# Kernel optimization log

Hardware: AMD Instinct MI355X
Metric: run time of the kernel (lower is better)

Reference implementation:

```python
import jax, jax.numpy as jnp
import numpy as np
from jax import lax

# --- config (matches init_kwargs) ---
D = 1024        # hidden_dim
H = 16          # num_heads
DH = D // H     # head dim
S = 5           # num_saccades
W = 128         # window_size
BK = 32         # block_size
TAU = 1.0       # gumbel temperature
DFF = 4 * D
EPS = 1e-5


def _ln(x, g, b):
    m = jnp.mean(x, axis=-1, keepdims=True)
    v = jnp.mean(jnp.square(x - m), axis=-1, keepdims=True)
    return (x - m) * lax.rsqrt(v + EPS) * g + b


def setup_inputs() -> dict:
    key = jax.random.key(0)
    ks = jax.random.split(key, 16)
    B, L = 4, 2048
    NB = L // BK
    sd = 0.02
    inp = {
        "hidden_states": jax.random.normal(ks[0], (B, L, D), jnp.float32),
        "gumbel_u": jax.random.uniform(ks[1], (S, B, NB), jnp.float32),
        "ln1_g": jnp.ones((D,), jnp.float32),
        "ln1_b": jnp.zeros((D,), jnp.float32),
        "ln2_g": jnp.ones((D,), jnp.float32),
        "ln2_b": jnp.zeros((D,), jnp.float32),
        "w_sal": jax.random.normal(ks[2], (D,), jnp.float32) * sd,
        "b_sal": jnp.zeros((), jnp.float32),
        "in_proj_w": jax.random.normal(ks[3], (3 * D, D), jnp.float32) * sd,
        "in_proj_b": jnp.zeros((3 * D,), jnp.float32),
        "out_proj_w": jax.random.normal(ks[4], (D, D), jnp.float32) * sd,
        "out_proj_b": jnp.zeros((D,), jnp.float32),
        "w_fc": jax.random.normal(ks[5], (D, DFF), jnp.float32) * sd,
        "b_fc": jnp.zeros((DFF,), jnp.float32),
        "w_proj": jax.random.normal(ks[6], (DFF, D), jnp.float32) * sd,
        "b_proj": jnp.zeros((D,), jnp.float32),
    }
    return inp


def reference(hidden_states, gumbel_u, ln1_g, ln1_b, ln2_g, ln2_b, w_sal, b_sal,
              in_proj_w, in_proj_b, out_proj_w, out_proj_b, w_fc, b_fc, w_proj, b_proj):
    x = hidden_states
    B, L, _ = x.shape
    NB = L // BK

    # ---- pre-norm ----
    h = _ln(x, ln1_g, ln1_b)

    # ---- peripheral map: mean-pool blocks, saliency logits ----
    blocks = h.reshape(B, NB, BK, D).mean(axis=2)          # (B, NB, D)
    logits = blocks @ w_sal + b_sal                        # (B, NB)

    # ---- gumbel-softmax hard block selection (straight-through) ----
    g = -jnp.log(-jnp.log(gumbel_u + 1e-9) + 1e-9)          # (S, B, NB)
    pert = (logits[None] + g) / TAU                         # (S, B, NB)
    p = jax.nn.softmax(pert, axis=-1)
    sel = jnp.argmax(pert, axis=-1)                         # (S, B) int
    w_soft = jnp.take_along_axis(p, sel[..., None], axis=-1)[..., 0]  # (S, B)
    scale = 1.0 + w_soft - lax.stop_gradient(w_soft)        # ST: fwd == 1

    # ---- gather fixation windows around selected block centers ----
    center = sel * BK + BK // 2
    start = jnp.clip(center - W // 2, 0, L - W)             # (S, B)
    idx = start[..., None] + jnp.arange(W)                  # (S, B, W)
    windows = h[jnp.arange(B)[None, :, None], idx, :]       # (S, B, W, D)
    windows = windows * scale[..., None, None]
    kv = windows.transpose(1, 0, 2, 3).reshape(B, S * W, D)  # (B, S*W, D)

    # ---- foveal MHA: queries = all tokens, keys/values = fixations ----
    wq, wk, wv = in_proj_w[:D], in_proj_w[D:2 * D], in_proj_w[2 * D:]
    bq, bk, bv = in_proj_b[:D], in_proj_b[D:2 * D], in_proj_b[2 * D:]
    q = (h @ wq.T + bq).reshape(B, L, H, DH)
    k = (kv @ wk.T + bk).reshape(B, S * W, H, DH)
    v = (kv @ wv.T + bv).reshape(B, S * W, H, DH)
    scores = jnp.einsum('blhd,bmhd->bhlm', q, k) / np.sqrt(DH).astype(np.float32)
    attn = jax.nn.softmax(scores, axis=-1)
    o = jnp.einsum('bhlm,bmhd->blhd', attn, v).reshape(B, L, D)
    o = o @ out_proj_w.T + out_proj_b

    x = x + o                                               # residual 1

    # ---- MLP (GPT-2: gelu-new) ----
    h2 = _ln(x, ln2_g, ln2_b)
    m = jax.nn.gelu(h2 @ w_fc + b_fc, approximate=True) @ w_proj + b_proj
    return x + m                                            # residual 2
```

## Files before the change

### kernel.cpp

```cpp
#include <hip/hip_runtime.h>

#define D_   1024
#define H_   16
#define DH_  64
#define S_   5
#define W_   128
#define BKB_ 32
#define DFF_ 4096
#define B_   4
#define L_   2048
#define NB_  64
#define SW_  (S_*W_)

typedef unsigned short u16;
typedef __attribute__((ext_vector_type(8))) short short8;
typedef __attribute__((ext_vector_type(4))) float floatx4;

__device__ __forceinline__ u16 f2bf(float f){
  unsigned int u = __float_as_uint(f);
  unsigned int r = 0x7fffu + ((u >> 16) & 1u);
  return (u16)((u + r) >> 16);
}

__device__ __forceinline__ void async_copy16(const u16* g, u16* lds){
  __builtin_amdgcn_global_load_lds(
      (const __attribute__((address_space(1))) void*)g,
      (__attribute__((address_space(3))) void*)lds, 16, 0, 0);
}

__device__ __forceinline__ float gelu_fast(float x){
  float u2 = 1.5957691216057308f * x * __builtin_fmaf(0.044715f, x*x, 1.0f);
  u2 = fminf(u2, 20.0f);
  float t = __expf(u2);
  return x * t * __builtin_amdgcn_rcpf(t + 1.0f);
}

__global__ void cast_f32_to_bf16(const float* __restrict__ in, u16* __restrict__ out, int n4){
  int i = blockIdx.x*256 + threadIdx.x;
  if (i < n4){
    float4 v = reinterpret_cast<const float4*>(in)[i];
    uint2 p;
    p.x = (unsigned)f2bf(v.x) | ((unsigned)f2bf(v.y) << 16);
    p.y = (unsigned)f2bf(v.z) | ((unsigned)f2bf(v.w) << 16);
    reinterpret_cast<uint2*>(out)[i] = p;
  }
}

__global__ void transpose_cast(const float* __restrict__ in, u16* __restrict__ out, int R, int C){
  __shared__ float t[32][33];
  int bx = blockIdx.x*32, by = blockIdx.y*32;
  int x = threadIdx.x & 31, y = threadIdx.x >> 5;
  #pragma unroll
  for (int i=0;i<4;i++)
    t[y + i*8][x] = in[(long long)(by + y + i*8)*C + bx + x];
  __syncthreads();
  #pragma unroll
  for (int i=0;i<4;i++)
    out[(long long)(bx + y + i*8)*R + by + x] = f2bf(t[x][y + i*8]);
}

template<bool ROWDOT>
__global__ __launch_bounds__(256) void ln_kernel(
    const float* __restrict__ x, const float* __restrict__ g, const float* __restrict__ b,
    const float* __restrict__ wsal, u16* __restrict__ out, float* __restrict__ logits)
{
  __shared__ float red[8];
  int row = blockIdx.x;
  int t = threadIdx.x;
  const float* xr = x + (long long)row*D_;
  float4 v = reinterpret_cast<const float4*>(xr)[t];
  float s  = v.x+v.y+v.z+v.w;
  float sq = v.x*v.x+v.y*v.y+v.z*v.z+v.w*v.w;
  #pragma unroll
  for (int m=32;m>=1;m>>=1){ s += __shfl_xor(s,m); sq += __shfl_xor(sq,m); }
  int wid = t>>6;
  if ((t&63)==0){ red[wid]=s; red[wid+4]=sq; }
  __syncthreads();
  s  = red[0]+red[1]+red[2]+red[3];
  sq = red[4]+red[5]+red[6]+red[7];
  float mean = s * (1.0f/D_);
  float var  = sq * (1.0f/D_) - mean*mean;
  float rstd = rsqrtf(fmaxf(var,0.0f) + 1e-5f);
  float4 gg = reinterpret_cast<const float4*>(g)[t];
  float4 bb = reinterpret_cast<const float4*>(b)[t];
  float h0 = (v.x-mean)*rstd*gg.x + bb.x;
  float h1 = (v.y-mean)*rstd*gg.y + bb.y;
  float h2 = (v.z-mean)*rstd*gg.z + bb.z;
  float h3 = (v.w-mean)*rstd*gg.w + bb.w;
  uint2 p;
  p.x = (unsigned)f2bf(h0) | ((unsigned)f2bf(h1) << 16);
  p.y = (unsigned)f2bf(h2) | ((unsigned)f2bf(h3) << 16);
  reinterpret_cast<uint2*>(out + (long long)row*D_)[t] = p;
  if (ROWDOT){
    float4 ww = reinterpret_cast<const float4*>(wsal)[t];
    float d = h0*ww.x + h1*ww.y + h2*ww.z + h3*ww.w;
    #pragma unroll
    for (int m=32;m>=1;m>>=1) d += __shfl_xor(d,m);
    __syncthreads();
    if ((t&63)==0) red[wid] = d;
    __syncthreads();
    if (t==0)
      atomicAdd(logits + (row>>5), (red[0]+red[1]+red[2]+red[3]) * (1.0f/BKB_));
  }
}

__global__ void select_kernel(const float* __restrict__ logits, const float* __restrict__ gum,
                              const float* __restrict__ bsal, int* __restrict__ start)
{
  int s = blockIdx.x >> 2, b = blockIdx.x & 3;
  int n = threadIdx.x;
  float u = gum[(s*B_ + b)*NB_ + n];
  float g = -logf(-logf(u + 1e-9f) + 1e-9f);
  float val = logits[b*NB_ + n] + bsal[0] + g;
  int idx = n;
  #pragma unroll
  for (int m=1;m<64;m<<=1){
    float ov = __shfl_xor(val, m);
    int   oi = __shfl_xor(idx, m);
    if (ov > val || (ov == val && oi < idx)) { val = ov; idx = oi; }
  }
  if (n==0){
    int c = idx*BKB_ + BKB_/2 - W_/2;
    c = c < 0 ? 0 : (c > (L_-W_) ? (L_-W_) : c);
    start[blockIdx.x] = c;
  }
}

__global__ void gather_kv(const u16* __restrict__ h, const int* __restrict__ start, u16* __restrict__ kv){
  int row = blockIdx.x;
  int b = row / SW_; int sw = row % SW_; int s = sw >> 7; int w = sw & 127;
  long long src = (long long)(b*L_ + start[s*B_ + b] + w)*D_;
  reinterpret_cast<uint2*>(kv + (long long)row*D_)[threadIdx.x] =
      reinterpret_cast<const uint2*>(h + src)[threadIdx.x];
}

template<int EPI>
__global__ __launch_bounds__(256) void gemm_bt(
    const u16* __restrict__ A, const u16* __restrict__ Bm,
    const float* __restrict__ bias, const float* __restrict__ res,
    void* __restrict__ Cout, void* __restrict__ Cout2, int M, int N, int K)
{
  __shared__ u16 As[2][128*32];
  __shared__ u16 Bs[2][128*32];
  const int tid = threadIdx.x;
  const int wave = tid>>6, lane = tid&63;
  const int wr = wave>>1, wc = wave&1;
  const int quad = lane>>4, l16 = lane&15;
  const int rowA0 = blockIdx.x*128;
  const int colB0 = blockIdx.y*128;
  const int r0  = tid>>2;
  const int cst = (tid&3) ^ ((tid>>2)&3);
  const u16* aP0 = A  + (long long)(rowA0 + r0     )*K + cst*8;
  const u16* aP1 = A  + (long long)(rowA0 + 64 + r0)*K + cst*8;
  const u16* bP0 = Bm + (long long)(colB0 + r0     )*K + cst*8;
  const u16* bP1 = Bm + (long long)(colB0 + 64 + r0)*K + cst*8;
  u16* ldsA = &As[0][0] + wave*512;
  u16* ldsB = &Bs[0][0] + wave*512;
  const int swq = l16 & 3;
  floatx4 acc[4][4];
  #pragma unroll
  for (int i=0;i<4;i++)
    #pragma unroll
    for (int j=0;j<4;j++) acc[i][j] = (floatx4)0.0f;

  const int T = K >> 5;
  async_copy16(aP0, ldsA);
  async_copy16(aP1, ldsA + 2048);
  async_copy16(bP0, ldsB);
  async_copy16(bP1, ldsB + 2048);

  for (int t=0; t<T; ++t){
    __syncthreads();
    if (t+1 < T){
      const int nb = (t+1)&1, ko = (t+1)<<5;
      async_copy16(aP0 + ko, ldsA + nb*4096);
      async_copy16(aP1 + ko, ldsA + nb*4096 + 2048);
      async_copy16(bP0 + ko, ldsB + nb*4096);
      async_copy16(bP1 + ko, ldsB + nb*4096 + 2048);
    }
    const u16* Ab = &As[t&1][0];
    const u16* Bb = &Bs[t&1][0];
    short8 af[4], bfv[4];
    #pragma unroll
    for (int i=0;i<4;i++){
      const int co = ((quad ^ swq))*8;
      af[i]  = *reinterpret_cast<const short8*>(Ab + (wr*64 + i*16 + l16)*32 + co);
      bfv[i] = *reinterpret_cast<const short8*>(Bb + (wc*64 + i*16 + l16)*32 + co);
    }
    #pragma unroll
    for (int i=0;i<4;i++)
      #pragma unroll
      for (int j=0;j<4;j++)
        acc[i][j] = __builtin_amdgcn_mfma_f32_16x16x32_bf16(af[i], bfv[j], acc[i][j], 0,0,0);
  }

  #pragma unroll
  for (int i=0;i<4;i++){
    #pragma unroll
    for (int j=0;j<4;j++){
      int row0 = rowA0 + wr*64 + i*16 + quad*4;
      int col  = colB0 + wc*64 + j*16 + l16;
      float bc = bias[col];
      if (EPI==3){
        if (col < 1024){
          #pragma unroll
          for (int r=0;r<4;r++)
            ((u16*)Cout)[(long long)(row0+r)*1024 + col] = f2bf(acc[i][j][r] + bc);
        } else {
          int vcol = col - 1024;
          int h = vcol >> 6, dh = vcol & 63;
          int b = row0 / SW_, mm = row0 % SW_;
          uint2 pk;
          pk.x = (unsigned)f2bf(acc[i][j][0]+bc) | ((unsigned)f2bf(acc[i][j][1]+bc) << 16);
          pk.y = (unsigned)f2bf(acc[i][j][2]+bc) | ((unsigned)f2bf(acc[i][j][3]+bc) << 16);
          *reinterpret_cast<uint2*>((u16*)Cout2 + ((long long)((b*H_ + h)*DH_ + dh))*SW_ + mm) = pk;
        }
      } else {
        #pragma unroll
        for (int r=0;r<4;r++){
          long long cidx = (long long)(row0+r)*N + col;
          float val = acc[i][j][r] + bc;
          if (EPI==0)      ((u16*)Cout)[cidx] = f2bf(val);
          else if (EPI==1) ((u16*)Cout)[cidx] = f2bf(gelu_fast(val));
          else             ((float*)Cout)[cidx] = val + res[cidx];
        }
      }
    }
  }
}

__global__ __launch_bounds__(256) void attn_kernel(
    const u16* __restrict__ q, const u16* __restrict__ k, const u16* __restrict__ vT,
    u16* __restrict__ o)
{
  const int bh = blockIdx.x;
  const int b = bh >> 4, h = bh & 15;
  const int tid = threadIdx.x;
  const int wave = tid >> 6, lane = tid & 63;
  const int quad = lane >> 4, l16 = lane & 15;
  const int qrow0 = blockIdx.y*64 + wave*16;

  __shared__ u16 Ks[64*64];
  __shared__ u16 Vs[64*64];
  __shared__ u16 Ps[4][16*72];

  const u16* qp = q + ((long long)(b*L_ + qrow0 + l16)*D_ + h*DH_ + quad*8);
  short8 qf0 = *reinterpret_cast<const short8*>(qp);
  short8 qf1 = *reinterpret_cast<const short8*>(qp + 32);

  floatx4 Oacc[4];
  #pragma unroll
  for (int dt=0;dt<4;dt++) Oacc[dt] = (floatx4)0.0f;
  float lsum = 0.0f;

  const int srow = lane >> 3;
  const int scol = ((lane & 7) ^ srow) * 8;
  const int sw16 = l16 & 7;
  u16* PsW = Ps[wave];

  for (int mt=0; mt<SW_/64; ++mt){
    const int m0 = mt*64;
    __syncthreads();
    #pragma unroll
    for (int c=0;c<2;c++){
      int rk = wave*8 + c*32 + srow;
      async_copy16(k  + ((long long)(b*SW_ + m0 + rk)*D_ + h*DH_) + scol,
                   Ks + (wave*8 + c*32)*64);
      async_copy16(vT + ((long long)(bh*DH_ + rk)*SW_ + m0) + scol,
                   Vs + (wave*8 + c*32)*64);
    }
    __syncthreads();

    #pragma unroll
    for (int sub=0; sub<4; ++sub){
      short8 kf0 = *reinterpret_cast<const short8*>(Ks + (sub*16+l16)*64 + ((quad  ) ^ sw16)*8);
      short8 kf1 = *reinterpret_cast<const short8*>(Ks + (sub*16+l16)*64 + ((quad+4) ^ sw16)*8);
      floatx4 st = (floatx4)0.0f;
      st = __builtin_amdgcn_mfma_f32_16x16x32_bf16(kf0, qf0, st, 0,0,0);
      st = __builtin_amdgcn_mfma_f32_16x16x32_bf16(kf1, qf1, st, 0,0,0);
      float p0 = __expf(st[0]*0.125f);
      float p1 = __expf(st[1]*0.125f);
      float p2 = __expf(st[2]*0.125f);
      float p3 = __expf(st[3]*0.125f);
      lsum += (p0+p1) + (p2+p3);
      uint2 pk;
      pk.x = (unsigned)f2bf(p0) | ((unsigned)f2bf(p1) << 16);
      pk.y = (unsigned)f2bf(p2) | ((unsigned)f2bf(p3) << 16);
      *reinterpret_cast<uint2*>(PsW + l16*72 + sub*16 + quad*4) = pk;
    }

    short8 pf0 = *reinterpret_cast<const short8*>(PsW + l16*72 + quad*8);
    short8 pf1 = *reinterpret_cast<const short8*>(PsW + l16*72 + 32 + quad*8);

    #pragma unroll
    for (int dt=0; dt<4; ++dt){
      short8 vf0 = *reinterpret_cast<const short8*>(Vs + (dt*16+l16)*64 + ((quad  ) ^ sw16)*8);
      short8 vf1 = *reinterpret_cast<const short8*>(Vs + (dt*16+l16)*64 + ((quad+4) ^ sw16)*8);
      Oacc[dt] = __builtin_amdgcn_mfma_f32_16x16x32_bf16(pf0, vf0, Oacc[dt], 0,0,0);
      Oacc[dt] = __builtin_amdgcn_mfma_f32_16x16x32_bf16(pf1, vf1, Oacc[dt], 0,0,0);
    }
  }

  lsum += __shfl_xor(lsum, 16);
  lsum += __shfl_xor(lsum, 32);

  #pragma unroll
  for (int r=0;r<4;r++){
    float linv = 1.0f / __shfl(lsum, quad*4 + r);
    int qrow = qrow0 + quad*4 + r;
    #pragma unroll
    for (int dt=0;dt<4;dt++)
      o[((long long)(b*L_ + qrow))*D_ + h*DH_ + dt*16 + l16] = f2bf(Oacc[dt][r]*linv);
  }
}

extern "C" void kernel_launch(void* const* d_in, const int* in_sizes, int n_in,
                              void* d_out, int out_size, void* d_ws, size_t ws_size,
                              hipStream_t stream)
{
  const float* x     = (const float*)d_in[0];
  const float* gum   = (const float*)d_in[1];
  const float* ln1g  = (const float*)d_in[2];
  const float* ln1b  = (const float*)d_in[3];
  const float* ln2g  = (const float*)d_in[4];
  const float* ln2b  = (const float*)d_in[5];
  const float* wsal  = (const float*)d_in[6];
  const float* bsal  = (const float*)d_in[7];
  const float* inpw  = (const float*)d_in[8];
  const float* inpb  = (const float*)d_in[9];
  const float* outw  = (const float*)d_in[10];
  const float* outb  = (const float*)d_in[11];
  const float* wfc   = (const float*)d_in[12];
  const float* bfc   = (const float*)d_in[13];
  const float* wproj = (const float*)d_in[14];
  const float* bproj = (const float*)d_in[15];
  float* outp = (float*)d_out;
  char* ws = (char*)d_ws;

  const size_t BLD2 = (size_t)B_*L_*D_*2;
  size_t off = 0;
  auto alloc = [&](size_t n){ char* p = ws + off; off += (n + 1023) & ~(size_t)1023; return p; };
  u16*  WfcT   = (u16*)alloc((size_t)DFF_*D_*2);
  u16*  WprojT = (u16*)alloc((size_t)D_*DFF_*2);
  float* x2    = (float*)alloc((size_t)B_*L_*D_*4);
  float* logits= (float*)alloc(B_*NB_*4);
  int*  startb = (int*)alloc(S_*B_*4);
  char* regA = ws + off;
  size_t o1 = 0;
  auto alloc1 = [&](size_t n){ char* p = regA + o1; o1 += (n + 1023) & ~(size_t)1023; return p; };
  u16* h_buf = (u16*)alloc1(BLD2);
  u16* Wqkv  = (u16*)alloc1((size_t)3*D_*D_*2);
  u16* Wout  = (u16*)alloc1((size_t)D_*D_*2);
  u16* qb    = (u16*)alloc1(BLD2);
  u16* kvb   = (u16*)alloc1((size_t)B_*SW_*D_*2);
  u16* kb    = (u16*)alloc1((size_t)B_*SW_*D_*2);
  u16* vTb   = (u16*)alloc1((size_t)B_*SW_*D_*2);
  u16* ob    = (u16*)alloc1(BLD2);
  u16* h2b = (u16*)regA;
  u16* act = (u16*)(regA + ((BLD2 + 1023) & ~(size_t)1023));

  hipMemsetAsync(logits, 0, B_*NB_*4, stream);

  cast_f32_to_bf16<<<3*D_*D_/1024, 256, 0, stream>>>(inpw, Wqkv, 3*D_*D_/4);
  cast_f32_to_bf16<<<D_*D_/1024,   256, 0, stream>>>(outw, Wout, D_*D_/4);
  transpose_cast<<<dim3(DFF_/32, D_/32), 256, 0, stream>>>(wfc,   WfcT,   D_,   DFF_);
  transpose_cast<<<dim3(D_/32, DFF_/32), 256, 0, stream>>>(wproj, WprojT, DFF_, D_);

  ln_kernel<true><<<B_*L_, 256, 0, stream>>>(x, ln1g, ln1b, wsal, h_buf, logits);
  select_kernel<<<S_*B_, 64, 0, stream>>>(logits, gum, bsal, startb);
  gather_kv<<<B_*SW_, 256, 0, stream>>>(h_buf, startb, kvb);

  gemm_bt<0><<<dim3(B_*L_/128,  D_/128), 256, 0, stream>>>(h_buf, Wqkv, inpb, nullptr, qb, nullptr, B_*L_, D_, D_);
  gemm_bt<3><<<dim3(B_*SW_/128, 2*D_/128), 256, 0, stream>>>(kvb, Wqkv + D_*D_, inpb + D_, nullptr, kb, vTb, B_*SW_, 2*D_, D_);

  attn_kernel<<<dim3(B_*H_, L_/64), 256, 0, stream>>>(qb, kb, vTb, ob);

  gemm_bt<2><<<dim3(B_*L_/128, D_/128), 256, 0, stream>>>(ob, Wout, outb, x, x2, nullptr, B_*L_, D_, D_);

  ln_kernel<false><<<B_*L_, 256, 0, stream>>>(x2, ln2g, ln2b, nullptr, h2b, nullptr);

  gemm_bt<1><<<dim3(B_*L_/128, DFF_/128), 256, 0, stream>>>(h2b, WfcT,   bfc,   nullptr, act,  nullptr, B_*L_, DFF_, D_);
  gemm_bt<2><<<dim3(B_*L_/128, D_/128),   256, 0, stream>>>(act, WprojT, bproj, x2,      outp, nullptr, B_*L_, D_,   DFF_);
}
```

Before: 497.3 us.

## Enlarge GEMM block tile to 256x128 with 8x4 MFMA accumulators per wave

The bf16 MFMA GEMM block tile grows from 128x128 to 256x128 rows. Each wave now computes a 128x64 sub-tile, loading each A fragment once and reusing the four B fragments across eight row tiles. The LDS swizzle and async-load mapping are reworked so each wave stages its own rows. All GEMM launches halve their grid size along M, and launch_bounds adds a minimum of 2 blocks. The aim is higher arithmetic intensity and less global and LDS traffic per FLOP. The cost is more accumulator registers, more LDS, and fewer blocks, so the smaller-N GEMMs get only about one block per CU.

```diff
diff --git a/kernel.cpp b/kernel.cpp
--- a/kernel.cpp
+++ b/kernel.cpp
@@ -135,70 +135,71 @@
 }
 
 template<int EPI>
-__global__ __launch_bounds__(256) void gemm_bt(
+__global__ __launch_bounds__(256, 2) void gemm_bt(
     const u16* __restrict__ A, const u16* __restrict__ Bm,
     const float* __restrict__ bias, const float* __restrict__ res,
     void* __restrict__ Cout, void* __restrict__ Cout2, int M, int N, int K)
 {
-  __shared__ u16 As[2][128*32];
+  __shared__ u16 As[2][256*32];
   __shared__ u16 Bs[2][128*32];
   const int tid = threadIdx.x;
   const int wave = tid>>6, lane = tid&63;
   const int wr = wave>>1, wc = wave&1;
   const int quad = lane>>4, l16 = lane&15;
-  const int rowA0 = blockIdx.x*128;
+  const int rowA0 = blockIdx.x*256;
   const int colB0 = blockIdx.y*128;
-  const int r0  = tid>>2;
-  const int cst = (tid&3) ^ ((tid>>2)&3);
-  const u16* aP0 = A  + (long long)(rowA0 + r0     )*K + cst*8;
-  const u16* aP1 = A  + (long long)(rowA0 + 64 + r0)*K + cst*8;
-  const u16* bP0 = Bm + (long long)(colB0 + r0     )*K + cst*8;
-  const u16* bP1 = Bm + (long long)(colB0 + 64 + r0)*K + cst*8;
-  u16* ldsA = &As[0][0] + wave*512;
-  u16* ldsB = &Bs[0][0] + wave*512;
-  const int swq = l16 & 3;
-  floatx4 acc[4][4];
-  #pragma unroll
-  for (int i=0;i<4;i++)
+  const int sub = lane>>2, pc = lane&3;
+  const int lc  = pc ^ ((sub ^ (sub>>2)) & 3);
+  const u16* aP = A  + (long long)(rowA0 + wave*64 + sub)*K + lc*8;
+  const u16* bP = Bm + (long long)(colB0 + wave*32 + sub)*K + lc*8;
+  const int cq = (quad ^ ((l16 ^ (l16>>2)) & 3)) * 8;
+
+  floatx4 acc[8][4];
+  #pragma unroll
+  for (int i=0;i<8;i++)
     #pragma unroll
     for (int j=0;j<4;j++) acc[i][j] = (floatx4)0.0f;
 
   const int T = K >> 5;
-  async_copy16(aP0, ldsA);
-  async_copy16(aP1, ldsA + 2048);
-  async_copy16(bP0, ldsB);
-  async_copy16(bP1, ldsB + 2048);
+  #pragma unroll
+  for (int g=0;g<4;g++)
+    async_copy16(aP + (long long)g*16*K, &As[0][0] + (wave*64 + g*16)*32);
+  #pragma unroll
+  for (int g=0;g<2;g++)
+    async_copy16(bP + (long long)g*16*K, &Bs[0][0] + (wave*32 + g*16)*32);
 
   for (int t=0; t<T; ++t){
     __syncthreads();
     if (t+1 < T){
-      const int nb = (t+1)&1, ko = (t+1)<<5;
-      async_copy16(aP0 + ko, ldsA + nb*4096);
-      async_copy16(aP1 + ko, ldsA + nb*4096 + 2048);
-      async_copy16(bP0 + ko, ldsB + nb*4096);
-      async_copy16(bP1 + ko, ldsB + nb*4096 + 2048);
+      const int nb = (t+1)&1;
+      const long long ko = (long long)(t+1)*32;
+      #pragma unroll
+      for (int g=0;g<4;g++)
+        async_copy16(aP + (long long)g*16*K + ko, &As[nb][0] + (wave*64 + g*16)*32);
+      #pragma unroll
+      for (int g=0;g<2;g++)
+        async_copy16(bP + (long long)g*16*K + ko, &Bs[nb][0] + (wave*32 + g*16)*32);
     }
     const u16* Ab = &As[t&1][0];
     const u16* Bb = &Bs[t&1][0];
-    short8 af[4], bfv[4];
-    #pragma unroll
-    for (int i=0;i<4;i++){
-      const int co = ((quad ^ swq))*8;
-      af[i]  = *reinterpret_cast<const short8*>(Ab + (wr*64 + i*16 + l16)*32 + co);
-      bfv[i] = *reinterpret_cast<const short8*>(Bb + (wc*64 + i*16 + l16)*32 + co);
-    }
-    #pragma unroll
-    for (int i=0;i<4;i++)
+    short8 bf[4];
+    #pragma unroll
+    for (int j=0;j<4;j++)
+      bf[j] = *reinterpret_cast<const short8*>(Bb + (wc*64 + j*16 + l16)*32 + cq);
+    #pragma unroll
+    for (int i=0;i<8;i++){
+      short8 af = *reinterpret_cast<const short8*>(Ab + (wr*128 + i*16 + l16)*32 + cq);
       #pragma unroll
       for (int j=0;j<4;j++)
-        acc[i][j] = __builtin_amdgcn_mfma_f32_16x16x32_bf16(af[i], bfv[j], acc[i][j], 0,0,0);
-  }
-
-  #pragma unroll
-  for (int i=0;i<4;i++){
+        acc[i][j] = __builtin_amdgcn_mfma_f32_16x16x32_bf16(af, bf[j], acc[i][j], 0,0,0);
+    }
+  }
+
+  #pragma unroll
+  for (int i=0;i<8;i++){
     #pragma unroll
     for (int j=0;j<4;j++){
-      int row0 = rowA0 + wr*64 + i*16 + quad*4;
+      int row0 = rowA0 + wr*128 + i*16 + quad*4;
       int col  = colB0 + wc*64 + j*16 + l16;
       float bc = bias[col];
       if (EPI==3){
@@ -370,15 +371,15 @@
   select_kernel<<<S_*B_, 64, 0, stream>>>(logits, gum, bsal, startb);
   gather_kv<<<B_*SW_, 256, 0, stream>>>(h_buf, startb, kvb);
 
-  gemm_bt<0><<<dim3(B_*L_/128,  D_/128), 256, 0, stream>>>(h_buf, Wqkv, inpb, nullptr, qb, nullptr, B_*L_, D_, D_);
-  gemm_bt<3><<<dim3(B_*SW_/128, 2*D_/128), 256, 0, stream>>>(kvb, Wqkv + D_*D_, inpb + D_, nullptr, kb, vTb, B_*SW_, 2*D_, D_);
+  gemm_bt<0><<<dim3(B_*L_/256,  D_/128), 256, 0, stream>>>(h_buf, Wqkv, inpb, nullptr, qb, nullptr, B_*L_, D_, D_);
+  gemm_bt<3><<<dim3(B_*SW_/256, 2*D_/128), 256, 0, stream>>>(kvb, Wqkv + D_*D_, inpb + D_, nullptr, kb, vTb, B_*SW_, 2*D_, D_);
 
   attn_kernel<<<dim3(B_*H_, L_/64), 256, 0, stream>>>(qb, kb, vTb, ob);
 
-  gemm_bt<2><<<dim3(B_*L_/128, D_/128), 256, 0, stream>>>(ob, Wout, outb, x, x2, nullptr, B_*L_, D_, D_);
+  gemm_bt<2><<<dim3(B_*L_/256, D_/128), 256, 0, stream>>>(ob, Wout, outb, x, x2, nullptr, B_*L_, D_, D_);
 
   ln_kernel<false><<<B_*L_, 256, 0, stream>>>(x2, ln2g, ln2b, nullptr, h2b, nullptr);
 
-  gemm_bt<1><<<dim3(B_*L_/128, DFF_/128), 256, 0, stream>>>(h2b, WfcT,   bfc,   nullptr, act,  nullptr, B_*L_, DFF_, D_);
-  gemm_bt<2><<<dim3(B_*L_/128, D_/128),   256, 0, stream>>>(act, WprojT, bproj, x2,      outp, nullptr, B_*L_, D_,   DFF_);
-}
+  gemm_bt<1><<<dim3(B_*L_/256, DFF_/128), 256, 0, stream>>>(h2b, WfcT,   bfc,   nullptr, act,  nullptr, B_*L_, DFF_, D_);
+  gemm_bt<2><<<dim3(B_*L_/256, D_/128),   256, 0, stream>>>(act, WprojT, bproj, x2,      outp, nullptr, B_*L_, D_,   DFF_);
+}
```

After: 563.5 us. 1.13x slower.
